# Optimization experiments

Hardware: AMD Instinct MI355X
Metric: run time of the kernel (lower is better)

The kernel has to match this reference:

```python
import jax, jax.numpy as jnp
import numpy as np

B, S, D, H = 1, 4096, 768, 12
W_HEAD = D // H  # 64


def setup_inputs() -> dict:
    key = jax.random.key(0)
    k1, k2, k3 = jax.random.split(key, 3)
    x = jax.random.normal(k1, (B, S, D), dtype=jnp.float32)
    mask = jnp.ones((B, S), dtype=jnp.float32)
    W_qkv = jax.random.normal(k2, (D, 3 * D), dtype=jnp.float32) * (1.0 / np.sqrt(D))
    b_qkv = jax.random.normal(k3, (3 * D,), dtype=jnp.float32) * 0.02
    return {"x": x, "mask": mask, "W_qkv": W_qkv, "b_qkv": b_qkv}


def reference(x, mask, W_qkv, b_qkv):
    # fused QKV projection: (B,S,D) @ (D,3D) -> (B,S,3D)
    qkv = jnp.einsum('bsd,de->bse', x, W_qkv) + b_qkv
    q, k, v = jnp.split(qkv, 3, axis=-1)
    # split heads: (B,S,D) -> (B,H,S,W)
    def to_heads(t):
        return t.reshape(B, S, H, W_HEAD).transpose(0, 2, 1, 3)
    q, k, v = to_heads(q), to_heads(k), to_heads(v)
    scores = jnp.einsum('bhsw,bhtw->bhst', q, k) / np.sqrt(W_HEAD)
    # additive mask: mask (B,S) -> (B,1,1,S); 1 = keep
    scores = scores - 10000.0 * (1.0 - mask[:, None, None, :])
    scores = jax.nn.softmax(scores, axis=-1)
    h = jnp.einsum('bhst,bhtw->bhsw', scores, v)
    # merge heads: (B,H,S,W) -> (B,S,D)
    h = h.transpose(0, 2, 1, 3).reshape(B, S, D)
    return h
```

## Files before the change

### kernel.cpp

```cpp
#include <hip/hip_runtime.h>
#include <hip/hip_bf16.h>

namespace {
constexpr int S  = 4096;
constexpr int D  = 768;
constexpr int H  = 12;
constexpr int N3 = 2304;

typedef __bf16 bf16x4 __attribute__((ext_vector_type(4)));
typedef __bf16 bf16x8 __attribute__((ext_vector_type(8)));
typedef float  floatx4 __attribute__((ext_vector_type(4)));

__device__ inline void glds16(const __bf16* g, __bf16* l) {
  __builtin_amdgcn_global_load_lds(
      (const __attribute__((address_space(1))) void*)(const void*)g,
      (__attribute__((address_space(3))) void*)(void*)l, 16, 0, 0);
}

__global__ __launch_bounds__(256)
void convert_all(const float* __restrict__ x, __bf16* __restrict__ xb,
                 const float* __restrict__ W, __bf16* __restrict__ WT)
{
  const int bid = blockIdx.x;
  const int tid = threadIdx.x;
  if (bid < 3072) {
    const int i = (bid * 256 + tid) * 4;
    floatx4 v = *reinterpret_cast<const floatx4*>(x + i);
    bf16x4 b;
    #pragma unroll
    for (int e = 0; e < 4; ++e) b[e] = (__bf16)v[e];
    *reinterpret_cast<bf16x4*>(xb + i) = b;
  } else {
    __shared__ float T[64][65];
    const int b2 = bid - 3072;
    const int d0 = (b2 % 12) * 64, e0 = (b2 / 12) * 64;
    const int rr = tid >> 4, c4 = (tid & 15) * 4;
    #pragma unroll
    for (int it = 0; it < 4; ++it) {
      int d = it * 16 + rr;
      floatx4 v = *reinterpret_cast<const floatx4*>(W + (d0 + d) * N3 + e0 + c4);
      #pragma unroll
      for (int e = 0; e < 4; ++e) T[d][c4 + e] = v[e];
    }
    __syncthreads();
    #pragma unroll
    for (int it = 0; it < 4; ++it) {
      int e = it * 16 + rr;
      bf16x4 b;
      #pragma unroll
      for (int i = 0; i < 4; ++i) b[i] = (__bf16)T[c4 + i][e];
      *reinterpret_cast<bf16x4*>(WT + (e0 + e) * D + d0 + c4) = b;
    }
  }
}

__global__ __launch_bounds__(256)
void qkv_gemm(const __bf16* __restrict__ xb, const __bf16* __restrict__ WT,
              const float* __restrict__ bq, __bf16* __restrict__ Qb,
              __bf16* __restrict__ Kb, __bf16* __restrict__ vT)
{
  __shared__ __bf16 smem[14336];
  __bf16* As = smem;
  __bf16* Bs = smem + 8192;

  const int tid  = threadIdx.x;
  const int wave = tid >> 6, lane = tid & 63;
  const int quad = lane >> 4, l16 = lane & 15;
  const int m_base = (wave >> 1) * 64;
  const int n_base = (wave & 1) * 48;
  const int bm = blockIdx.x, bn = blockIdx.y;
  const int srow = lane >> 3, sg = lane & 7;

  floatx4 acc[4][3];
  #pragma unroll
  for (int i = 0; i < 4; ++i)
    #pragma unroll
    for (int j = 0; j < 3; ++j) acc[i][j] = (floatx4){0.f, 0.f, 0.f, 0.f};

  for (int ks = 0; ks < 12; ++ks) {
    const int k0 = ks * 64;
    __syncthreads();
    #pragma unroll
    for (int it = 0; it < 4; ++it) {
      int rbase = it * 32 + wave * 8;
      int row = rbase + srow;
      glds16(xb + (size_t)(bm * 128 + row) * D + k0 + (sg ^ (row & 7)) * 8,
             As + rbase * 64);
    }
    #pragma unroll
    for (int it = 0; it < 3; ++it) {
      int rbase = it * 32 + wave * 8;
      int row = rbase + srow;
      glds16(WT + (size_t)(bn * 96 + row) * D + k0 + (sg ^ (row & 7)) * 8,
             Bs + rbase * 64);
    }
    __syncthreads();

    bf16x8 af[4][2], bfr[3][2];
    #pragma unroll
    for (int mt = 0; mt < 4; ++mt)
      #pragma unroll
      for (int kt = 0; kt < 2; ++kt) {
        int m = m_base + mt * 16 + l16;
        af[mt][kt] = *reinterpret_cast<const bf16x8*>(
            &As[m * 64 + ((((kt << 2) | quad) ^ (l16 & 7)) << 3)]);
      }
    #pragma unroll
    for (int nt = 0; nt < 3; ++nt)
      #pragma unroll
      for (int kt = 0; kt < 2; ++kt) {
        int n = n_base + nt * 16 + l16;
        bfr[nt][kt] = *reinterpret_cast<const bf16x8*>(
            &Bs[n * 64 + ((((kt << 2) | quad) ^ (l16 & 7)) << 3)]);
      }
    #pragma unroll
    for (int kt = 0; kt < 2; ++kt)
      #pragma unroll
      for (int mt = 0; mt < 4; ++mt)
        #pragma unroll
        for (int nt = 0; nt < 3; ++nt)
          acc[mt][nt] = __builtin_amdgcn_mfma_f32_16x16x32_bf16(
              af[mt][kt], bfr[nt][kt], acc[mt][nt], 0, 0, 0);
  }

  if (bn < 16) {
    #pragma unroll
    for (int nt = 0; nt < 3; ++nt) {
      int col = bn * 96 + n_base + nt * 16 + l16;
      float bias = bq[col];
      #pragma unroll
      for (int mt = 0; mt < 4; ++mt) {
        int row = bm * 128 + m_base + mt * 16 + quad * 4;
        #pragma unroll
        for (int r = 0; r < 4; ++r) {
          __bf16 v = (__bf16)(acc[mt][nt][r] + bias);
          if (bn < 8) Qb[(row + r) * D + col] = v;
          else        Kb[(row + r) * D + (col - D)] = v;
        }
      }
    }
  } else {
    __syncthreads();
    __bf16* vts = smem;
    #pragma unroll
    for (int nt = 0; nt < 3; ++nt) {
      int wl = n_base + nt * 16 + l16;
      float bias = bq[bn * 96 + wl];
      int sw = (wl & 7) << 3;
      #pragma unroll
      for (int mt = 0; mt < 4; ++mt) {
        #pragma unroll
        for (int r = 0; r < 4; ++r) {
          int tl = m_base + mt * 16 + quad * 4 + r;
          int pos = (tl & ~31) | (quad << 3) | ((tl & 16) >> 2) | r;
          vts[wl * 128 + (pos ^ sw)] = (__bf16)(acc[mt][nt][r] + bias);
        }
      }
    }
    __syncthreads();
    const int w0g = bn * 96 - 2 * D;
    #pragma unroll
    for (int it = 0; it < 6; ++it) {
      int c = it * 256 + tid;
      int wl = c >> 4, t0 = (c & 15) * 8;
      bf16x8 v = *reinterpret_cast<const bf16x8*>(
          &vts[wl * 128 + (t0 ^ ((wl & 7) << 3))]);
      *reinterpret_cast<bf16x8*>(
          &vT[(size_t)(w0g + wl) * S + bm * 128 + t0]) = v;
    }
  }
}

__global__ __launch_bounds__(256)
void attention(const __bf16* __restrict__ Qb, const __bf16* __restrict__ Kb,
               const __bf16* __restrict__ vT, const float* __restrict__ mask,
               float* __restrict__ out)
{
  __shared__ char smem[49408];
  __bf16* Vt = (__bf16*)(smem + 32768);
  float*  Ll = (float*)(smem + 49152);
  float*  Lo = (float*)smem;

  const int tid  = threadIdx.x;
  const int wave = tid >> 6, lane = tid & 63;
  const int quad = lane >> 4, l16 = lane & 15;
  const int qh = wave >> 1;
  const int th = wave & 1;
  const int qb = blockIdx.x, h = blockIdx.y;
  const int q0 = qb * 64;
  const int qcol = h * 64;
  const int srow = lane >> 3, sg = lane & 7;
  const int vrow = lane >> 4, vs = lane & 15;

  bf16x8 qf[2][2];
  #pragma unroll
  for (int nt = 0; nt < 2; ++nt)
    #pragma unroll
    for (int kt = 0; kt < 2; ++kt)
      qf[nt][kt] = *reinterpret_cast<const bf16x8*>(
          Qb + (q0 + qh * 32 + nt * 16 + l16) * D + qcol + kt * 32 + quad * 8);

  floatx4 accO[4][2];
  #pragma unroll
  for (int wt = 0; wt < 4; ++wt)
    #pragma unroll
    for (int nt = 0; nt < 2; ++nt) accO[wt][nt] = (floatx4){0.f, 0.f, 0.f, 0.f};
  floatx4 accL[2];
  accL[0] = (floatx4){0.f, 0.f, 0.f, 0.f};
  accL[1] = (floatx4){0.f, 0.f, 0.f, 0.f};
  bf16x8 ones;
  #pragma unroll
  for (int e = 0; e < 8; ++e) ones[e] = (__bf16)1.0f;

  auto stageK = [&](int j, __bf16* dst) {
    #pragma unroll
    for (int it = 0; it < 4; ++it) {
      int rbase = it * 32 + wave * 8;
      int t = rbase + srow;
      glds16(Kb + (size_t)(j * 128 + t) * D + qcol + (sg ^ (t & 7)) * 8,
             dst + rbase * 64);
    }
  };
  auto stageV = [&](int j) {
    #pragma unroll
    for (int it = 0; it < 4; ++it) {
      int wbase = it * 16 + wave * 4;
      int w = wbase + vrow;
      glds16(vT + (size_t)(qcol + w) * S + j * 128 + (vs ^ (w & 7)) * 8,
             Vt + wbase * 128);
    }
  };

  stageK(0, (__bf16*)smem);
  stageV(0);

  for (int j = 0; j < 32; ++j) {
    floatx4 mv[4];
    #pragma unroll
    for (int mt = 0; mt < 4; ++mt)
      mv[mt] = *reinterpret_cast<const floatx4*>(
          mask + j * 128 + th * 64 + mt * 16 + quad * 4);

    asm volatile("s_waitcnt vmcnt(8)" ::: "memory");
    __builtin_amdgcn_s_barrier();
    __builtin_amdgcn_sched_barrier(0);

    if (j < 31)
      stageK(j + 1, (__bf16*)(smem + (((j + 1) & 1) << 14)));
    __builtin_amdgcn_sched_barrier(0);

    const __bf16* Kc = (const __bf16*)(smem + ((j & 1) << 14));

    bf16x4 ps[4][2];
    #pragma unroll
    for (int mt = 0; mt < 4; ++mt) {
      int trow = th * 64 + mt * 16 + l16;
      bf16x8 kf[2];
      #pragma unroll
      for (int kt = 0; kt < 2; ++kt)
        kf[kt] = *reinterpret_cast<const bf16x8*>(
            &Kc[trow * 64 + ((((kt << 2) | quad) ^ (l16 & 7)) << 3)]);
      floatx4 am;
      #pragma unroll
      for (int r = 0; r < 4; ++r)
        am[r] = fmaf(mv[mt][r], 14426.9504f, -14426.9504f);
      #pragma unroll
      for (int nt = 0; nt < 2; ++nt) {
        floatx4 s = (floatx4){0.f, 0.f, 0.f, 0.f};
        #pragma unroll
        for (int kt = 0; kt < 2; ++kt)
          s = __builtin_amdgcn_mfma_f32_16x16x32_bf16(kf[kt], qf[nt][kt], s, 0, 0, 0);
        #pragma unroll
        for (int r = 0; r < 4; ++r)
          ps[mt][nt][r] = (__bf16)__builtin_amdgcn_exp2f(
              fmaf(s[r], 0.18033688f, am[r]));
      }
    }

    asm volatile("s_waitcnt vmcnt(4)" ::: "memory");
    __builtin_amdgcn_s_barrier();
    __builtin_amdgcn_sched_barrier(0);

    #pragma unroll
    for (int u = 0; u < 2; ++u) {
      bf16x8 pf[2];
      #pragma unroll
      for (int nt = 0; nt < 2; ++nt)
        #pragma unroll
        for (int r = 0; r < 4; ++r) {
          pf[nt][r]     = ps[2 * u][nt][r];
          pf[nt][4 + r] = ps[2 * u + 1][nt][r];
        }
      #pragma unroll
      for (int nt = 0; nt < 2; ++nt)
        accL[nt] = __builtin_amdgcn_mfma_f32_16x16x32_bf16(
            ones, pf[nt], accL[nt], 0, 0, 0);
      #pragma unroll
      for (int wt = 0; wt < 4; ++wt) {
        int w = wt * 16 + l16;
        bf16x8 vf = *reinterpret_cast<const bf16x8*>(
            &Vt[w * 128 + (((th * 8 + u * 4 + quad) ^ (w & 7)) << 3)]);
        #pragma unroll
        for (int nt = 0; nt < 2; ++nt)
          accO[wt][nt] = __builtin_amdgcn_mfma_f32_16x16x32_bf16(
              vf, pf[nt], accO[wt][nt], 0, 0, 0);
      }
    }

    __builtin_amdgcn_s_barrier();
    __builtin_amdgcn_sched_barrier(0);
    if (j < 31) stageV(j + 1);
    __builtin_amdgcn_sched_barrier(0);
  }

  float l_lane[2] = {accL[0][0], accL[1][0]};

  __syncthreads();
  if (th == 1) {
    float* dst = Lo + qh * (64 * 33);
    #pragma unroll
    for (int wt = 0; wt < 4; ++wt)
      #pragma unroll
      for (int nt = 0; nt < 2; ++nt)
        #pragma unroll
        for (int r = 0; r < 4; ++r)
          dst[(wt * 16 + quad * 4 + r) * 33 + nt * 16 + l16] = accO[wt][nt][r];
    if (quad == 0) {
      #pragma unroll
      for (int nt = 0; nt < 2; ++nt)
        Ll[qh * 32 + nt * 16 + l16] = l_lane[nt];
    }
  }
  __syncthreads();
  if (th == 0) {
    const float* src = Lo + qh * (64 * 33);
    float l_tot[2];
    #pragma unroll
    for (int nt = 0; nt < 2; ++nt)
      l_tot[nt] = l_lane[nt] + Ll[qh * 32 + nt * 16 + l16];
    #pragma unroll
    for (int wt = 0; wt < 4; ++wt)
      #pragma unroll
      for (int nt = 0; nt < 2; ++nt) {
        floatx4 o;
        #pragma unroll
        for (int r = 0; r < 4; ++r)
          o[r] = (accO[wt][nt][r] +
                  src[(wt * 16 + quad * 4 + r) * 33 + nt * 16 + l16]) / l_tot[nt];
        int row = q0 + qh * 32 + nt * 16 + l16;
        int col = qcol + wt * 16 + quad * 4;
        *reinterpret_cast<floatx4*>(&out[row * D + col]) = o;
      }
  }
}

}

extern "C" void kernel_launch(void* const* d_in, const int* in_sizes, int n_in,
                              void* d_out, int out_size, void* d_ws, size_t ws_size,
                              hipStream_t stream) {
  const float *x = nullptr, *mask = nullptr, *Wq = nullptr, *bq = nullptr;
  for (int i = 0; i < n_in; ++i) {
    switch (in_sizes[i]) {
      case 3145728: x    = (const float*)d_in[i]; break;
      case 4096:    mask = (const float*)d_in[i]; break;
      case 1769472: Wq   = (const float*)d_in[i]; break;
      case 2304:    bq   = (const float*)d_in[i]; break;
      default: break;
    }
  }

  __bf16* xb = (__bf16*)d_out;
  __bf16* WT = xb + (size_t)S * D;
  __bf16* Qb = (__bf16*)d_ws;
  __bf16* Kb = Qb + (size_t)S * D;
  __bf16* vT = Kb + (size_t)S * D;

  convert_all<<<3072 + 432, 256, 0, stream>>>(x, xb, Wq, WT);
  qkv_gemm   <<<dim3(S / 128, N3 / 96), 256, 0, stream>>>(xb, WT, bq, Qb, Kb, vT);
  attention  <<<dim3(S / 64, H), 256, 0, stream>>>(Qb, Kb, vT, mask, (float*)d_out);
}
```

Baseline: 169.2 us.

## Split attention key tiles across four waves per query half with 512-thread blocks

The attention kernel moves from 256 to 512 threads per block. Each query half is now handled by four waves, and each wave covers 32 keys of every 128-key tile instead of 64. K/V staging is spread over the eight waves and the wait counts are adjusted to match. The epilogue now reduces three partial O and L accumulators through a larger LDS buffer instead of one. The aim is more waves in flight to hide latency and shorter per-wave dependency chains, at the cost of a bigger cross-wave reduction and more LDS use.

```diff
diff --git a/kernel.cpp b/kernel.cpp
--- a/kernel.cpp
+++ b/kernel.cpp
@@ -171,21 +171,19 @@
   }
 }
 
-__global__ __launch_bounds__(256)
+__global__ __launch_bounds__(512, 6)
 void attention(const __bf16* __restrict__ Qb, const __bf16* __restrict__ Kb,
                const __bf16* __restrict__ vT, const float* __restrict__ mask,
                float* __restrict__ out)
 {
-  __shared__ char smem[49408];
+  __shared__ char smem[51456];
   __bf16* Vt = (__bf16*)(smem + 32768);
-  float*  Ll = (float*)(smem + 49152);
-  float*  Lo = (float*)smem;
 
   const int tid  = threadIdx.x;
   const int wave = tid >> 6, lane = tid & 63;
   const int quad = lane >> 4, l16 = lane & 15;
-  const int qh = wave >> 1;
-  const int th = wave & 1;
+  const int qh = wave >> 2;
+  const int th = wave & 3;
   const int qb = blockIdx.x, h = blockIdx.y;
   const int q0 = qb * 64;
   const int qcol = h * 64;
@@ -214,8 +212,8 @@
 
   auto stageK = [&](int j, __bf16* dst) {
     #pragma unroll
-    for (int it = 0; it < 4; ++it) {
-      int rbase = it * 32 + wave * 8;
+    for (int it = 0; it < 2; ++it) {
+      int rbase = it * 64 + wave * 8;
       int t = rbase + srow;
       glds16(Kb + (size_t)(j * 128 + t) * D + qcol + (sg ^ (t & 7)) * 8,
              dst + rbase * 64);
@@ -223,25 +221,27 @@
   };
   auto stageV = [&](int j) {
     #pragma unroll
-    for (int it = 0; it < 4; ++it) {
-      int wbase = it * 16 + wave * 4;
+    for (int it = 0; it < 2; ++it) {
+      int wbase = it * 32 + wave * 4;
       int w = wbase + vrow;
       glds16(vT + (size_t)(qcol + w) * S + j * 128 + (vs ^ (w & 7)) * 8,
              Vt + wbase * 128);
     }
   };
 
+  __builtin_amdgcn_sched_barrier(0);
   stageK(0, (__bf16*)smem);
   stageV(0);
+  __builtin_amdgcn_sched_barrier(0);
 
   for (int j = 0; j < 32; ++j) {
-    floatx4 mv[4];
-    #pragma unroll
-    for (int mt = 0; mt < 4; ++mt)
+    floatx4 mv[2];
+    #pragma unroll
+    for (int mt = 0; mt < 2; ++mt)
       mv[mt] = *reinterpret_cast<const floatx4*>(
-          mask + j * 128 + th * 64 + mt * 16 + quad * 4);
-
-    asm volatile("s_waitcnt vmcnt(8)" ::: "memory");
+          mask + j * 128 + th * 32 + mt * 16 + quad * 4);
+
+    asm volatile("s_waitcnt vmcnt(4)" ::: "memory");
     __builtin_amdgcn_s_barrier();
     __builtin_amdgcn_sched_barrier(0);
 
@@ -251,10 +251,10 @@
 
     const __bf16* Kc = (const __bf16*)(smem + ((j & 1) << 14));
 
-    bf16x4 ps[4][2];
-    #pragma unroll
-    for (int mt = 0; mt < 4; ++mt) {
-      int trow = th * 64 + mt * 16 + l16;
+    bf16x8 pf[2];
+    #pragma unroll
+    for (int mt = 0; mt < 2; ++mt) {
+      int trow = th * 32 + mt * 16 + l16;
       bf16x8 kf[2];
       #pragma unroll
       for (int kt = 0; kt < 2; ++kt)
@@ -272,39 +272,28 @@
           s = __builtin_amdgcn_mfma_f32_16x16x32_bf16(kf[kt], qf[nt][kt], s, 0, 0, 0);
         #pragma unroll
         for (int r = 0; r < 4; ++r)
-          ps[mt][nt][r] = (__bf16)__builtin_amdgcn_exp2f(
+          pf[nt][mt * 4 + r] = (__bf16)__builtin_amdgcn_exp2f(
               fmaf(s[r], 0.18033688f, am[r]));
       }
     }
 
-    asm volatile("s_waitcnt vmcnt(4)" ::: "memory");
+    asm volatile("s_waitcnt vmcnt(2)" ::: "memory");
     __builtin_amdgcn_s_barrier();
     __builtin_amdgcn_sched_barrier(0);
 
     #pragma unroll
-    for (int u = 0; u < 2; ++u) {
-      bf16x8 pf[2];
+    for (int nt = 0; nt < 2; ++nt)
+      accL[nt] = __builtin_amdgcn_mfma_f32_16x16x32_bf16(
+          ones, pf[nt], accL[nt], 0, 0, 0);
+    #pragma unroll
+    for (int wt = 0; wt < 4; ++wt) {
+      int w = wt * 16 + l16;
+      bf16x8 vf = *reinterpret_cast<const bf16x8*>(
+          &Vt[w * 128 + (((th * 4 + quad) ^ (w & 7)) << 3)]);
       #pragma unroll
       for (int nt = 0; nt < 2; ++nt)
-        #pragma unroll
-        for (int r = 0; r < 4; ++r) {
-          pf[nt][r]     = ps[2 * u][nt][r];
-          pf[nt][4 + r] = ps[2 * u + 1][nt][r];
-        }
-      #pragma unroll
-      for (int nt = 0; nt < 2; ++nt)
-        accL[nt] = __builtin_amdgcn_mfma_f32_16x16x32_bf16(
-            ones, pf[nt], accL[nt], 0, 0, 0);
-      #pragma unroll
-      for (int wt = 0; wt < 4; ++wt) {
-        int w = wt * 16 + l16;
-        bf16x8 vf = *reinterpret_cast<const bf16x8*>(
-            &Vt[w * 128 + (((th * 8 + u * 4 + quad) ^ (w & 7)) << 3)]);
-        #pragma unroll
-        for (int nt = 0; nt < 2; ++nt)
-          accO[wt][nt] = __builtin_amdgcn_mfma_f32_16x16x32_bf16(
-              vf, pf[nt], accO[wt][nt], 0, 0, 0);
-      }
+        accO[wt][nt] = __builtin_amdgcn_mfma_f32_16x16x32_bf16(
+            vf, pf[nt], accO[wt][nt], 0, 0, 0);
     }
 
     __builtin_amdgcn_s_barrier();
@@ -315,9 +304,11 @@
 
   float l_lane[2] = {accL[0][0], accL[1][0]};
 
+  float* Lo = (float*)smem;
+  float* Ll = (float*)(smem + 50688);
   __syncthreads();
-  if (th == 1) {
-    float* dst = Lo + qh * (64 * 33);
+  if (th != 0) {
+    float* dst = Lo + (qh * 3 + th - 1) * 2112;
     #pragma unroll
     for (int wt = 0; wt < 4; ++wt)
       #pragma unroll
@@ -328,25 +319,33 @@
     if (quad == 0) {
       #pragma unroll
       for (int nt = 0; nt < 2; ++nt)
-        Ll[qh * 32 + nt * 16 + l16] = l_lane[nt];
+        Ll[(qh * 3 + th - 1) * 32 + nt * 16 + l16] = l_lane[nt];
     }
   }
   __syncthreads();
   if (th == 0) {
-    const float* src = Lo + qh * (64 * 33);
     float l_tot[2];
     #pragma unroll
-    for (int nt = 0; nt < 2; ++nt)
-      l_tot[nt] = l_lane[nt] + Ll[qh * 32 + nt * 16 + l16];
+    for (int nt = 0; nt < 2; ++nt) {
+      l_tot[nt] = l_lane[nt];
+      #pragma unroll
+      for (int p = 0; p < 3; ++p)
+        l_tot[nt] += Ll[(qh * 3 + p) * 32 + nt * 16 + l16];
+    }
     #pragma unroll
     for (int wt = 0; wt < 4; ++wt)
       #pragma unroll
       for (int nt = 0; nt < 2; ++nt) {
         floatx4 o;
         #pragma unroll
-        for (int r = 0; r < 4; ++r)
-          o[r] = (accO[wt][nt][r] +
-                  src[(wt * 16 + quad * 4 + r) * 33 + nt * 16 + l16]) / l_tot[nt];
+        for (int r = 0; r < 4; ++r) {
+          float v = accO[wt][nt][r];
+          #pragma unroll
+          for (int p = 0; p < 3; ++p)
+            v += Lo[(qh * 3 + p) * 2112 +
+                    (wt * 16 + quad * 4 + r) * 33 + nt * 16 + l16];
+          o[r] = v / l_tot[nt];
+        }
         int row = q0 + qh * 32 + nt * 16 + l16;
         int col = qcol + wt * 16 + quad * 4;
         *reinterpret_cast<floatx4*>(&out[row * D + col]) = o;
@@ -378,5 +377,5 @@
 
   convert_all<<<3072 + 432, 256, 0, stream>>>(x, xb, Wq, WT);
   qkv_gemm   <<<dim3(S / 128, N3 / 96), 256, 0, stream>>>(xb, WT, bq, Qb, Kb, vT);
-  attention  <<<dim3(S / 64, H), 256, 0, stream>>>(Qb, Kb, vT, mask, (float*)d_out);
-}
+  attention  <<<dim3(S / 64, H), 512, 0, stream>>>(Qb, Kb, vT, mask, (float*)d_out);
+}
```

Result: slower. 424.4 us (+150.8%).

## Load V fragments straight from global into registers, bypassing LDS staging

Applied to the files above, without the earlier changes.

V tiles are no longer staged into shared memory through async global-to-LDS copies. Each wave now loads its V MFMA operands directly from global memory into registers, prefetching the next tile at the end of each iteration. This drops the V LDS buffer, its extra barrier and its LDS read traffic, and shrinks static shared memory from about 48 KB to 32 KB, which may allow more resident blocks per CU. The softmax probabilities are also written straight into the packed MFMA operand layout instead of being repacked. In exchange it holds 32 more VGPRs and issues less coalesced 16-byte global reads per lane, which rely on caching.

```diff
diff --git a/kernel.cpp b/kernel.cpp
--- a/kernel.cpp
+++ b/kernel.cpp
@@ -176,10 +176,7 @@
                const __bf16* __restrict__ vT, const float* __restrict__ mask,
                float* __restrict__ out)
 {
-  __shared__ char smem[49408];
-  __bf16* Vt = (__bf16*)(smem + 32768);
-  float*  Ll = (float*)(smem + 49152);
-  float*  Lo = (float*)smem;
+  __shared__ char smem[32768];
 
   const int tid  = threadIdx.x;
   const int wave = tid >> 6, lane = tid & 63;
@@ -190,7 +187,6 @@
   const int q0 = qb * 64;
   const int qcol = h * 64;
   const int srow = lane >> 3, sg = lane & 7;
-  const int vrow = lane >> 4, vs = lane & 15;
 
   bf16x8 qf[2][2];
   #pragma unroll
@@ -221,18 +217,22 @@
              dst + rbase * 64);
     }
   };
-  auto stageV = [&](int j) {
-    #pragma unroll
-    for (int it = 0; it < 4; ++it) {
-      int wbase = it * 16 + wave * 4;
-      int w = wbase + vrow;
-      glds16(vT + (size_t)(qcol + w) * S + j * 128 + (vs ^ (w & 7)) * 8,
-             Vt + wbase * 128);
-    }
+
+  bf16x8 vf[2][4];
+  auto loadV = [&](int j) {
+    #pragma unroll
+    for (int u = 0; u < 2; ++u)
+      #pragma unroll
+      for (int wt = 0; wt < 4; ++wt)
+        vf[u][wt] = *reinterpret_cast<const bf16x8*>(
+            vT + (size_t)(qcol + wt * 16 + l16) * S + j * 128
+               + (th * 8 + u * 4 + quad) * 8);
   };
 
   stageK(0, (__bf16*)smem);
-  stageV(0);
+  __builtin_amdgcn_sched_barrier(0);
+  loadV(0);
+  __builtin_amdgcn_sched_barrier(0);
 
   for (int j = 0; j < 32; ++j) {
     floatx4 mv[4];
@@ -240,8 +240,9 @@
     for (int mt = 0; mt < 4; ++mt)
       mv[mt] = *reinterpret_cast<const floatx4*>(
           mask + j * 128 + th * 64 + mt * 16 + quad * 4);
-
-    asm volatile("s_waitcnt vmcnt(8)" ::: "memory");
+    __builtin_amdgcn_sched_barrier(0);
+
+    asm volatile("s_waitcnt vmcnt(12)" ::: "memory");
     __builtin_amdgcn_s_barrier();
     __builtin_amdgcn_sched_barrier(0);
 
@@ -251,7 +252,7 @@
 
     const __bf16* Kc = (const __bf16*)(smem + ((j & 1) << 14));
 
-    bf16x4 ps[4][2];
+    bf16x8 pf[2][2];
     #pragma unroll
     for (int mt = 0; mt < 4; ++mt) {
       int trow = th * 64 + mt * 16 + l16;
@@ -272,49 +273,34 @@
           s = __builtin_amdgcn_mfma_f32_16x16x32_bf16(kf[kt], qf[nt][kt], s, 0, 0, 0);
         #pragma unroll
         for (int r = 0; r < 4; ++r)
-          ps[mt][nt][r] = (__bf16)__builtin_amdgcn_exp2f(
+          pf[mt >> 1][nt][(mt & 1) * 4 + r] = (__bf16)__builtin_amdgcn_exp2f(
               fmaf(s[r], 0.18033688f, am[r]));
       }
     }
 
-    asm volatile("s_waitcnt vmcnt(4)" ::: "memory");
-    __builtin_amdgcn_s_barrier();
-    __builtin_amdgcn_sched_barrier(0);
-
     #pragma unroll
     for (int u = 0; u < 2; ++u) {
-      bf16x8 pf[2];
-      #pragma unroll
-      for (int nt = 0; nt < 2; ++nt)
-        #pragma unroll
-        for (int r = 0; r < 4; ++r) {
-          pf[nt][r]     = ps[2 * u][nt][r];
-          pf[nt][4 + r] = ps[2 * u + 1][nt][r];
-        }
       #pragma unroll
       for (int nt = 0; nt < 2; ++nt)
         accL[nt] = __builtin_amdgcn_mfma_f32_16x16x32_bf16(
-            ones, pf[nt], accL[nt], 0, 0, 0);
-      #pragma unroll
-      for (int wt = 0; wt < 4; ++wt) {
-        int w = wt * 16 + l16;
-        bf16x8 vf = *reinterpret_cast<const bf16x8*>(
-            &Vt[w * 128 + (((th * 8 + u * 4 + quad) ^ (w & 7)) << 3)]);
+            ones, pf[u][nt], accL[nt], 0, 0, 0);
+      #pragma unroll
+      for (int wt = 0; wt < 4; ++wt)
         #pragma unroll
         for (int nt = 0; nt < 2; ++nt)
           accO[wt][nt] = __builtin_amdgcn_mfma_f32_16x16x32_bf16(
-              vf, pf[nt], accO[wt][nt], 0, 0, 0);
-      }
-    }
-
-    __builtin_amdgcn_s_barrier();
-    __builtin_amdgcn_sched_barrier(0);
-    if (j < 31) stageV(j + 1);
+              vf[u][wt], pf[u][nt], accO[wt][nt], 0, 0, 0);
+    }
+
+    __builtin_amdgcn_sched_barrier(0);
+    if (j < 31) loadV(j + 1);
     __builtin_amdgcn_sched_barrier(0);
   }
 
   float l_lane[2] = {accL[0][0], accL[1][0]};
 
+  float* Lo = (float*)smem;
+  float* Ll = (float*)(smem + 16896);
   __syncthreads();
   if (th == 1) {
     float* dst = Lo + qh * (64 * 33);
```

Result: slower. 229.1 us (+35.4%).
